# Performance work log

Measured on AMD Instinct MI355X. Metric: run time of the kernel, lower is better.

## Reference

```python
import jax, jax.numpy as jnp
import numpy as np

H = 1024       # hidden_size
E = 1024       # embedding_size
V = 50257      # output_size (vocab)
L = 64         # max_length


def setup_inputs() -> dict:
    key = jax.random.key(0)
    ks = jax.random.split(key, 12)
    s = 0.02
    return {
        "input": jax.random.randint(ks[0], (1,), 0, V),
        "hidden": jax.random.normal(ks[1], (1, 1, H), dtype=jnp.float32),
        "encoder_outputs": jax.random.normal(ks[2], (L, H), dtype=jnp.float32),
        "emb": jax.random.normal(ks[3], (V, E), dtype=jnp.float32) * s,
        "attn_w": jax.random.normal(ks[4], (L, H + E), dtype=jnp.float32) * s,
        "attn_b": jnp.zeros((L,), dtype=jnp.float32),
        "comb_w": jax.random.normal(ks[5], (E, H + E), dtype=jnp.float32) * s,
        "comb_b": jnp.zeros((E,), dtype=jnp.float32),
        "w_ih": jax.random.normal(ks[6], (3 * H, E), dtype=jnp.float32) * s,
        "b_ih": jnp.zeros((3 * H,), dtype=jnp.float32),
        "w_hh": jax.random.normal(ks[7], (3 * H, H), dtype=jnp.float32) * s,
        "b_hh": jnp.zeros((3 * H,), dtype=jnp.float32),
        "out_w": jax.random.normal(ks[8], (V, H), dtype=jnp.float32) * s,
        "out_b": jnp.zeros((V,), dtype=jnp.float32),
    }


def reference(input, hidden, encoder_outputs, emb, attn_w, attn_b,
              comb_w, comb_b, w_ih, b_ih, w_hh, b_hh, out_w, out_b):
    # embedding + (dropout = identity in eval)
    embedded = emb[input].reshape(1, E)            # [1, E]
    h0 = hidden[0]                                  # [1, H]
    # Bahdanau-style attention over fixed-length encoder outputs
    attn_logits = jnp.concatenate([embedded, h0], axis=1) @ attn_w.T + attn_b
    attn_weights = jax.nn.softmax(attn_logits, axis=1)      # [1, L]
    attn_applied = attn_weights @ encoder_outputs            # [1, H]
    x = jnp.concatenate([embedded, attn_applied], axis=1) @ comb_w.T + comb_b
    x = jax.nn.relu(x)                               # [1, E]
    # single GRU cell step (torch gate order: r, z, n)
    gi = x @ w_ih.T + b_ih
    gh = h0 @ w_hh.T + b_hh
    i_r, i_z, i_n = jnp.split(gi, 3, axis=1)
    h_r, h_z, h_n = jnp.split(gh, 3, axis=1)
    r = jax.nn.sigmoid(i_r + h_r)
    z = jax.nn.sigmoid(i_z + h_z)
    n = jnp.tanh(i_n + r * h_n)
    h_new = (1.0 - z) * n + z * h0                   # [1, H]
    logp = jax.nn.log_softmax(h_new @ out_w.T + out_b, axis=1)  # [1, V]
    return logp, h_new[None], attn_weights
```

## Files before the change

### kernel.cpp

```cpp
#include <hip/hip_runtime.h>
#include <math.h>

#define H 1024
#define E 1024
#define V 50257
#define L 64
#define HE 2048

typedef float floatx4 __attribute__((ext_vector_type(4)));

__device__ inline float dot4(float4 a, float4 b) {
    return a.x*b.x + a.y*b.y + a.z*b.z + a.w*b.w;
}

__device__ inline floatx4 ldnt(const float4* p) {
    return __builtin_nontemporal_load((const floatx4*)p);
}

__device__ inline float dotn(floatx4 a, float4 b) {
    return a[0]*b.x + a[1]*b.y + a[2]*b.z + a[3]*b.w;
}

__device__ inline float wave_reduce_sum(float v) {
    #pragma unroll
    for (int off = 32; off > 0; off >>= 1)
        v += __shfl_down(v, off, 64);
    return v;
}

__global__ __launch_bounds__(512) void k_front(
        const int* __restrict__ inp,
        const float* __restrict__ hidden,
        const float* __restrict__ enc,
        const float* __restrict__ emb,
        const float* __restrict__ attn_w,
        const float* __restrict__ attn_b,
        const float* __restrict__ comb_w,
        const float* __restrict__ comb_b,
        const float* __restrict__ w_hh,
        const float* __restrict__ b_hh,
        float* __restrict__ x,
        float* __restrict__ gh,
        float* __restrict__ out_weights) {
    const int bid  = blockIdx.x;
    const int t    = threadIdx.x;
    const int wave = t >> 6;
    const int lane = t & 63;

    __shared__ float lgS[L];
    __shared__ float sig[L];
    __shared__ __align__(16) float aa[H];

    const float* erow = emb + (size_t)inp[0] * E;
    const float4* e4 = (const float4*)erow;
    const float4* h4 = (const float4*)hidden;

    if (bid < 128) {
        float4 ev[4], hv[4];
        #pragma unroll
        for (int i = 0; i < 4; ++i) { ev[i] = e4[i * 64 + lane]; hv[i] = h4[i * 64 + lane]; }
        float s[8];
        #pragma unroll
        for (int r = 0; r < 8; ++r) {
            int row = wave * 8 + r;
            const float4* w = (const float4*)(attn_w + (size_t)row * HE);
            float acc = 0.f;
            #pragma unroll
            for (int i = 0; i < 4; ++i) acc += dot4(w[i * 64 + lane], ev[i]);
            #pragma unroll
            for (int i = 0; i < 4; ++i) acc += dot4(w[256 + i * 64 + lane], hv[i]);
            s[r] = acc;
        }
        #pragma unroll
        for (int r = 0; r < 8; ++r) s[r] = wave_reduce_sum(s[r]);
        if (lane == 0) {
            #pragma unroll
            for (int r = 0; r < 8; ++r) {
                int row = wave * 8 + r;
                lgS[row] = s[r] + attn_b[row];
            }
        }
        __syncthreads();
        if (t < 64) {
            float v = lgS[t];
            float m = v;
            #pragma unroll
            for (int off = 32; off > 0; off >>= 1) m = fmaxf(m, __shfl_xor(m, off, 64));
            float ex = expf(v - m);
            float ssum = ex;
            #pragma unroll
            for (int off = 32; off > 0; off >>= 1) ssum += __shfl_xor(ssum, off, 64);
            float w = ex / ssum;
            sig[t] = w;
            if (bid == 0) out_weights[t] = w;
        }
        __syncthreads();
        {
            float a0 = 0.f, a1 = 0.f;
            #pragma unroll 8
            for (int l = 0; l < L; ++l) {
                float sl = sig[l];
                a0 += sl * enc[l * H + t];
                a1 += sl * enc[l * H + t + 512];
            }
            aa[t] = a0;
            aa[t + 512] = a1;
        }
        __syncthreads();
        {
            int row = bid * 8 + wave;
            const float4* wr = (const float4*)(comb_w + (size_t)row * HE);
            const float4* a4 = (const float4*)aa;
            float acc = 0.f;
            #pragma unroll
            for (int i = 0; i < 4; ++i) acc += dotn(ldnt(&wr[i * 64 + lane]), ev[i]);
            #pragma unroll
            for (int i = 0; i < 4; ++i) acc += dotn(ldnt(&wr[256 + i * 64 + lane]), a4[i * 64 + lane]);
            acc = wave_reduce_sum(acc);
            if (lane == 0) x[row] = fmaxf(acc + comb_b[row], 0.f);
        }
    } else {
        int row = (bid - 128) * 8 + wave;
        float4 hv[4];
        #pragma unroll
        for (int i = 0; i < 4; ++i) hv[i] = h4[i * 64 + lane];
        const float4* wr = (const float4*)(w_hh + (size_t)row * H);
        float acc = 0.f;
        #pragma unroll
        for (int i = 0; i < 4; ++i) acc += dotn(ldnt(&wr[i * 64 + lane]), hv[i]);
        acc = wave_reduce_sum(acc);
        if (lane == 0) gh[row] = acc + b_hh[row];
    }
}

__global__ __launch_bounds__(768) void k_gru(
        const float* __restrict__ x,
        const float* __restrict__ hidden,
        const float* __restrict__ w_ih,
        const float* __restrict__ b_ih,
        const float* __restrict__ gh,
        float* __restrict__ h_new) {
    int t = threadIdx.x, wave = t >> 6, lane = t & 63;
    int g  = wave >> 2;
    int j4 = wave & 3;
    int j  = blockIdx.x * 4 + j4;
    const float4* x4 = (const float4*)x;
    const float4* wr = (const float4*)(w_ih + (size_t)(g * H + j) * E);
    float s = 0.f;
    #pragma unroll
    for (int i = 0; i < 4; ++i)
        s += dotn(ldnt(&wr[i * 64 + lane]), x4[i * 64 + lane]);
    s = wave_reduce_sum(s);
    __shared__ float red[3][4];
    if (lane == 0) red[g][j4] = s + b_ih[g * H + j];
    __syncthreads();
    if (t < 4) {
        int jo = blockIdx.x * 4 + t;
        float i_r = red[0][t], i_z = red[1][t], i_n = red[2][t];
        float h_r = gh[jo], h_z = gh[H + jo], h_n = gh[2 * H + jo];
        float r = 1.f / (1.f + expf(-(i_r + h_r)));
        float z = 1.f / (1.f + expf(-(i_z + h_z)));
        float n = tanhf(i_n + r * h_n);
        h_new[jo] = (1.f - z) * n + z * hidden[jo];
    }
}

__global__ __launch_bounds__(256) void k_vocab(
        const float* __restrict__ h_new,
        const float* __restrict__ out_w,
        const float* __restrict__ out_b,
        float* __restrict__ logp,
        float* __restrict__ partials) {
    int t = threadIdx.x, wave = t >> 6, lane = t & 63;
    const float4* h4 = (const float4*)h_new;
    float4 hv[4];
    #pragma unroll
    for (int i = 0; i < 4; ++i) hv[i] = h4[i * 64 + lane];
    int base = blockIdx.x * 16 + wave * 4;
    float s[4] = {0.f, 0.f, 0.f, 0.f};
    if (base + 3 < V) {
        const float4* w0 = (const float4*)(out_w + (size_t)(base + 0) * H);
        const float4* w1 = (const float4*)(out_w + (size_t)(base + 1) * H);
        const float4* w2 = (const float4*)(out_w + (size_t)(base + 2) * H);
        const float4* w3 = (const float4*)(out_w + (size_t)(base + 3) * H);
        #pragma unroll
        for (int i = 0; i < 4; ++i) {
            int idx = i * 64 + lane;
            s[0] += dot4(w0[idx], hv[i]);
            s[1] += dot4(w1[idx], hv[i]);
            s[2] += dot4(w2[idx], hv[i]);
            s[3] += dot4(w3[idx], hv[i]);
        }
    } else {
        #pragma unroll
        for (int k = 0; k < 4; ++k)
            if (base + k < V) {
                const float4* w = (const float4*)(out_w + (size_t)(base + k) * H);
                #pragma unroll
                for (int i = 0; i < 4; ++i) s[k] += dot4(w[i * 64 + lane], hv[i]);
            }
    }
    #pragma unroll
    for (int off = 32; off > 0; off >>= 1) {
        s[0] += __shfl_down(s[0], off, 64);
        s[1] += __shfl_down(s[1], off, 64);
        s[2] += __shfl_down(s[2], off, 64);
        s[3] += __shfl_down(s[3], off, 64);
    }
    __shared__ float smP[4];
    if (lane == 0) {
        float pe = 0.f;
        #pragma unroll
        for (int k = 0; k < 4; ++k) {
            int r = base + k;
            if (r < V) {
                float v = s[k] + out_b[r];
                logp[r] = v;
                pe += expf(v);
            }
        }
        smP[wave] = pe;
    }
    __syncthreads();
    if (t == 0)
        partials[blockIdx.x] = smP[0] + smP[1] + smP[2] + smP[3];
}

__global__ __launch_bounds__(256) void k_lsm(
        float* __restrict__ logp,
        const float* __restrict__ partials, int nb) {
    int t = threadIdx.x;
    float S = 0.f;
    for (int i = t; i < nb; i += 256) S += partials[i];
    S = wave_reduce_sum(S);
    __shared__ float ss[4];
    __shared__ float sh_lz;
    if ((t & 63) == 0) ss[t >> 6] = S;
    __syncthreads();
    if (t == 0) sh_lz = logf(ss[0] + ss[1] + ss[2] + ss[3]);
    __syncthreads();
    float lz = sh_lz;
    int i = blockIdx.x * 256 + t;
    if (i < V) logp[i] -= lz;
}

extern "C" void kernel_launch(void* const* d_in, const int* in_sizes, int n_in,
                              void* d_out, int out_size, void* d_ws, size_t ws_size,
                              hipStream_t stream) {
    const int*   inp     = (const int*)d_in[0];
    const float* hidden  = (const float*)d_in[1];
    const float* enc     = (const float*)d_in[2];
    const float* emb     = (const float*)d_in[3];
    const float* attn_w  = (const float*)d_in[4];
    const float* attn_b  = (const float*)d_in[5];
    const float* comb_w  = (const float*)d_in[6];
    const float* comb_b  = (const float*)d_in[7];
    const float* w_ih    = (const float*)d_in[8];
    const float* b_ih    = (const float*)d_in[9];
    const float* w_hh    = (const float*)d_in[10];
    const float* b_hh    = (const float*)d_in[11];
    const float* out_w   = (const float*)d_in[12];
    const float* out_b   = (const float*)d_in[13];

    float* out          = (float*)d_out;
    float* logp         = out;
    float* h_new        = out + V;
    float* attn_weights = out + V + H;

    float* ws       = (float*)d_ws;
    float* gh       = ws;
    float* x        = ws + 3072;
    float* partials = ws + 4096;
    const int nb = (V + 15) / 16;

    k_front<<<512, 512, 0, stream>>>(inp, hidden, enc, emb, attn_w, attn_b,
                                     comb_w, comb_b, w_hh, b_hh,
                                     x, gh, attn_weights);
    k_gru<<<256, 768, 0, stream>>>(x, hidden, w_ih, b_ih, gh, h_new);
    k_vocab<<<nb, 256, 0, stream>>>(h_new, out_w, out_b, logp, partials);
    k_lsm<<<(V + 255) / 256, 256, 0, stream>>>(logp, partials, nb);
}
```

Baseline: 70.44 us.

## Move hidden-to-hidden GEMV from front kernel into GRU kernel, drop nontemporal loads

After: 70.13 us. Within noise of the previous version (-0.4%).

```diff
diff --git a/kernel.cpp b/kernel.cpp
--- a/kernel.cpp
+++ b/kernel.cpp
@@ -7,18 +7,8 @@
 #define L 64
 #define HE 2048
 
-typedef float floatx4 __attribute__((ext_vector_type(4)));
-
 __device__ inline float dot4(float4 a, float4 b) {
     return a.x*b.x + a.y*b.y + a.z*b.z + a.w*b.w;
-}
-
-__device__ inline floatx4 ldnt(const float4* p) {
-    return __builtin_nontemporal_load((const floatx4*)p);
-}
-
-__device__ inline float dotn(floatx4 a, float4 b) {
-    return a[0]*b.x + a[1]*b.y + a[2]*b.z + a[3]*b.w;
 }
 
 __device__ inline float wave_reduce_sum(float v) {
@@ -37,10 +27,7 @@
         const float* __restrict__ attn_b,
         const float* __restrict__ comb_w,
         const float* __restrict__ comb_b,
-        const float* __restrict__ w_hh,
-        const float* __restrict__ b_hh,
         float* __restrict__ x,
-        float* __restrict__ gh,
         float* __restrict__ out_weights) {
     const int bid  = blockIdx.x;
     const int t    = threadIdx.x;
@@ -55,81 +42,69 @@
     const float4* e4 = (const float4*)erow;
     const float4* h4 = (const float4*)hidden;
 
-    if (bid < 128) {
-        float4 ev[4], hv[4];
-        #pragma unroll
-        for (int i = 0; i < 4; ++i) { ev[i] = e4[i * 64 + lane]; hv[i] = h4[i * 64 + lane]; }
-        float s[8];
+    float4 ev[4], hv[4];
+    #pragma unroll
+    for (int i = 0; i < 4; ++i) { ev[i] = e4[i * 64 + lane]; hv[i] = h4[i * 64 + lane]; }
+
+    float s[8];
+    #pragma unroll
+    for (int r = 0; r < 8; ++r) {
+        int row = wave * 8 + r;
+        const float4* w = (const float4*)(attn_w + (size_t)row * HE);
+        float acc = 0.f;
+        #pragma unroll
+        for (int i = 0; i < 4; ++i) acc += dot4(w[i * 64 + lane], ev[i]);
+        #pragma unroll
+        for (int i = 0; i < 4; ++i) acc += dot4(w[256 + i * 64 + lane], hv[i]);
+        s[r] = acc;
+    }
+    #pragma unroll
+    for (int r = 0; r < 8; ++r) s[r] = wave_reduce_sum(s[r]);
+    if (lane == 0) {
         #pragma unroll
         for (int r = 0; r < 8; ++r) {
             int row = wave * 8 + r;
-            const float4* w = (const float4*)(attn_w + (size_t)row * HE);
-            float acc = 0.f;
-            #pragma unroll
-            for (int i = 0; i < 4; ++i) acc += dot4(w[i * 64 + lane], ev[i]);
-            #pragma unroll
-            for (int i = 0; i < 4; ++i) acc += dot4(w[256 + i * 64 + lane], hv[i]);
-            s[r] = acc;
-        }
-        #pragma unroll
-        for (int r = 0; r < 8; ++r) s[r] = wave_reduce_sum(s[r]);
-        if (lane == 0) {
-            #pragma unroll
-            for (int r = 0; r < 8; ++r) {
-                int row = wave * 8 + r;
-                lgS[row] = s[r] + attn_b[row];
-            }
-        }
-        __syncthreads();
-        if (t < 64) {
-            float v = lgS[t];
-            float m = v;
-            #pragma unroll
-            for (int off = 32; off > 0; off >>= 1) m = fmaxf(m, __shfl_xor(m, off, 64));
-            float ex = expf(v - m);
-            float ssum = ex;
-            #pragma unroll
-            for (int off = 32; off > 0; off >>= 1) ssum += __shfl_xor(ssum, off, 64);
-            float w = ex / ssum;
-            sig[t] = w;
-            if (bid == 0) out_weights[t] = w;
-        }
-        __syncthreads();
-        {
-            float a0 = 0.f, a1 = 0.f;
-            #pragma unroll 8
-            for (int l = 0; l < L; ++l) {
-                float sl = sig[l];
-                a0 += sl * enc[l * H + t];
-                a1 += sl * enc[l * H + t + 512];
-            }
-            aa[t] = a0;
-            aa[t + 512] = a1;
-        }
-        __syncthreads();
-        {
-            int row = bid * 8 + wave;
-            const float4* wr = (const float4*)(comb_w + (size_t)row * HE);
-            const float4* a4 = (const float4*)aa;
-            float acc = 0.f;
-            #pragma unroll
-            for (int i = 0; i < 4; ++i) acc += dotn(ldnt(&wr[i * 64 + lane]), ev[i]);
-            #pragma unroll
-            for (int i = 0; i < 4; ++i) acc += dotn(ldnt(&wr[256 + i * 64 + lane]), a4[i * 64 + lane]);
-            acc = wave_reduce_sum(acc);
-            if (lane == 0) x[row] = fmaxf(acc + comb_b[row], 0.f);
-        }
-    } else {
-        int row = (bid - 128) * 8 + wave;
-        float4 hv[4];
-        #pragma unroll
-        for (int i = 0; i < 4; ++i) hv[i] = h4[i * 64 + lane];
-        const float4* wr = (const float4*)(w_hh + (size_t)row * H);
+            lgS[row] = s[r] + attn_b[row];
+        }
+    }
+    __syncthreads();
+    if (t < 64) {
+        float v = lgS[t];
+        float m = v;
+        #pragma unroll
+        for (int off = 32; off > 0; off >>= 1) m = fmaxf(m, __shfl_xor(m, off, 64));
+        float ex = expf(v - m);
+        float ssum = ex;
+        #pragma unroll
+        for (int off = 32; off > 0; off >>= 1) ssum += __shfl_xor(ssum, off, 64);
+        float w = ex / ssum;
+        sig[t] = w;
+        if (bid == 0) out_weights[t] = w;
+    }
+    __syncthreads();
+    {
+        float a0 = 0.f, a1 = 0.f;
+        #pragma unroll 8
+        for (int l = 0; l < L; ++l) {
+            float sl = sig[l];
+            a0 += sl * enc[l * H + t];
+            a1 += sl * enc[l * H + t + 512];
+        }
+        aa[t] = a0;
+        aa[t + 512] = a1;
+    }
+    __syncthreads();
+    {
+        int row = bid * 8 + wave;
+        const float4* wr = (const float4*)(comb_w + (size_t)row * HE);
+        const float4* a4 = (const float4*)aa;
         float acc = 0.f;
         #pragma unroll
-        for (int i = 0; i < 4; ++i) acc += dotn(ldnt(&wr[i * 64 + lane]), hv[i]);
+        for (int i = 0; i < 4; ++i) acc += dot4(wr[i * 64 + lane], ev[i]);
+        #pragma unroll
+        for (int i = 0; i < 4; ++i) acc += dot4(wr[256 + i * 64 + lane], a4[i * 64 + lane]);
         acc = wave_reduce_sum(acc);
-        if (lane == 0) gh[row] = acc + b_hh[row];
+        if (lane == 0) x[row] = fmaxf(acc + comb_b[row], 0.f);
     }
 }
 
@@ -138,26 +113,39 @@
         const float* __restrict__ hidden,
         const float* __restrict__ w_ih,
         const float* __restrict__ b_ih,
-        const float* __restrict__ gh,
+        const float* __restrict__ w_hh,
+        const float* __restrict__ b_hh,
         float* __restrict__ h_new) {
     int t = threadIdx.x, wave = t >> 6, lane = t & 63;
     int g  = wave >> 2;
     int j4 = wave & 3;
     int j  = blockIdx.x * 4 + j4;
     const float4* x4 = (const float4*)x;
-    const float4* wr = (const float4*)(w_ih + (size_t)(g * H + j) * E);
-    float s = 0.f;
-    #pragma unroll
-    for (int i = 0; i < 4; ++i)
-        s += dotn(ldnt(&wr[i * 64 + lane]), x4[i * 64 + lane]);
-    s = wave_reduce_sum(s);
-    __shared__ float red[3][4];
-    if (lane == 0) red[g][j4] = s + b_ih[g * H + j];
+    const float4* h4 = (const float4*)hidden;
+    const float4* wi = (const float4*)(w_ih + (size_t)(g * H + j) * E);
+    const float4* wh = (const float4*)(w_hh + (size_t)(g * H + j) * H);
+    float si = 0.f, sh = 0.f;
+    #pragma unroll
+    for (int i = 0; i < 4; ++i) {
+        int idx = i * 64 + lane;
+        si += dot4(wi[idx], x4[idx]);
+        sh += dot4(wh[idx], h4[idx]);
+    }
+    #pragma unroll
+    for (int off = 32; off > 0; off >>= 1) {
+        si += __shfl_down(si, off, 64);
+        sh += __shfl_down(sh, off, 64);
+    }
+    __shared__ float redI[3][4], redH[3][4];
+    if (lane == 0) {
+        redI[g][j4] = si + b_ih[g * H + j];
+        redH[g][j4] = sh + b_hh[g * H + j];
+    }
     __syncthreads();
     if (t < 4) {
         int jo = blockIdx.x * 4 + t;
-        float i_r = red[0][t], i_z = red[1][t], i_n = red[2][t];
-        float h_r = gh[jo], h_z = gh[H + jo], h_n = gh[2 * H + jo];
+        float i_r = redI[0][t], i_z = redI[1][t], i_n = redI[2][t];
+        float h_r = redH[0][t], h_z = redH[1][t], h_n = redH[2][t];
         float r = 1.f / (1.f + expf(-(i_r + h_r)));
         float z = 1.f / (1.f + expf(-(i_z + h_z)));
         float n = tanhf(i_n + r * h_n);
@@ -268,15 +256,13 @@
     float* attn_weights = out + V + H;
 
     float* ws       = (float*)d_ws;
-    float* gh       = ws;
-    float* x        = ws + 3072;
-    float* partials = ws + 4096;
+    float* x        = ws;
+    float* partials = ws + 1024;
     const int nb = (V + 15) / 16;
 
-    k_front<<<512, 512, 0, stream>>>(inp, hidden, enc, emb, attn_w, attn_b,
-                                     comb_w, comb_b, w_hh, b_hh,
-                                     x, gh, attn_weights);
-    k_gru<<<256, 768, 0, stream>>>(x, hidden, w_ih, b_ih, gh, h_new);
+    k_front<<<128, 512, 0, stream>>>(inp, hidden, enc, emb, attn_w, attn_b,
+                                     comb_w, comb_b, x, attn_weights);
+    k_gru<<<256, 768, 0, stream>>>(x, hidden, w_ih, b_ih, w_hh, b_hh, h_new);
     k_vocab<<<nb, 256, 0, stream>>>(h_new, out_w, out_b, logp, partials);
     k_lsm<<<(V + 255) / 256, 256, 0, stream>>>(logp, partials, nb);
 }
```
